# Optimization experiments

Measured on AMD Instinct MI355X. Metric: run time of the kernel, lower is better.

The kernel has to match this reference:

```python
import jax, jax.numpy as jnp
import numpy as np

B, T, D = 16, 4096, 64
K = 4096              # num_embeddings
DECAY = 0.99
COMMITMENT = 0.25
EPS = 1e-5


def setup_inputs() -> dict:
    key = jax.random.key(0)
    k1, k2 = jax.random.split(key)
    inputs = jax.random.normal(k1, (B, T, D), dtype=jnp.float32)
    # torch init: uniform_(-1/K, 1/K); _ema_w initialized to a copy of weight
    weight = jax.random.uniform(k2, (K, D), dtype=jnp.float32, minval=-1.0 / K, maxval=1.0 / K)
    return {
        "inputs": inputs,
        "weight": weight,
        "ema_cluster_size": jnp.zeros((K,), jnp.float32),
        "ema_w": weight,
    }


def reference(inputs, weight, ema_cluster_size, ema_w):
    b, t, d = inputs.shape
    flat = inputs.reshape(-1, d)                                   # [N, D]
    dist = (jnp.sum(flat * flat, axis=1, keepdims=True)
            + jnp.sum(weight * weight, axis=1)
            - 2.0 * flat @ weight.T)
    idx = jnp.argmin(dist, axis=1)                                 # [N]
    quantized = weight[idx].reshape(inputs.shape)                  # gather [B,T,D]

    # --- EMA codebook update (torch.no_grad path; one-hot matmuls == segment sums) ---
    counts = jax.ops.segment_sum(jnp.ones((flat.shape[0],), flat.dtype), idx, num_segments=K)
    cs = ema_cluster_size * DECAY + (1.0 - DECAY) * counts
    n = jnp.sum(cs)
    cs = (cs + EPS) / (n + K * EPS) * n                            # Laplace smoothing
    dw = jax.ops.segment_sum(flat, idx, num_segments=K)            # encodings.T @ flat
    new_ema_w = ema_w * DECAY + (1.0 - DECAY) * dw
    new_weight = new_ema_w / cs[:, None]

    # --- losses (on pre-update codebook, as in torch) ---
    e_latent = jnp.mean((jax.lax.stop_gradient(quantized) - inputs) ** 2)
    q_latent = jnp.mean((quantized - jax.lax.stop_gradient(inputs)) ** 2)
    loss = q_latent + COMMITMENT * e_latent

    # straight-through estimator
    quantized_st = inputs + jax.lax.stop_gradient(quantized - inputs)
    encoding_indices = idx.reshape(b, t)
    return quantized_st, loss, encoding_indices, new_weight, cs, new_ema_w
```

## Files before the change

kernel.cpp:

```cpp
#include <hip/hip_runtime.h>
#include <math.h>

#define NROWS 65536
#define DDIM  64
#define KCODE 4096
#define NSPLIT 4
#define KSPL  (KCODE / NSPLIT)
#define STEPS (KSPL / 16)
#define SMASK (STEPS - 1)

#define O_Q    0
#define O_LOSS 4194304
#define O_IDX  4194305
#define O_NW   4259841
#define O_CS   4521985
#define O_NEW  4526081

#define O_A      262144
#define O_B2     327680
#define O_CNT   1000000
#define O_OFF   1010000
#define O_CUR   1020000
#define O_ORD   1030000
#define O_LP    (O_NW + 131074)

typedef _Float16 f16x8 __attribute__((ext_vector_type(8)));
typedef float    f32x4 __attribute__((ext_vector_type(4)));

__global__ __launch_bounds__(256)
void vq_prep(const float* __restrict__ x, const float* __restrict__ w,
             float* __restrict__ out, unsigned long long* __restrict__ keys) {
    int i = blockIdx.x * 256 + threadIdx.x;
    {
        const int k = i >> 6, j = i & 63;
        float E = w[i] * 4096.0f;
        _Float16 h = (_Float16)E;
        float r = E - (float)h;
        _Float16 lo = (_Float16)(r * 4096.0f);
        const size_t pos = (size_t)(k >> 4) * 1024 + (size_t)(j >> 5) * 512
                         + (size_t)((j >> 3) & 3) * 128 + (size_t)(k & 15) * 8
                         + (size_t)(j & 7);
        ((_Float16*)out)[pos] = h;
        ((_Float16*)out)[262144 + pos] = lo;
    }
    if (i < NROWS) keys[i] = 0xFFFFFFFFFFFFFFFFULL;
    if (i < KCODE) ((unsigned*)(out + O_CNT))[i] = 0u;
    if ((i & 3) == 0) {
        const int row = i >> 2;
        const float4* xr = (const float4*)(x + (size_t)row * DDIM);
        float ax = 0.f, ay = 0.f, az = 0.f, aw = 0.f;
        #pragma unroll
        for (int j = 0; j < 16; ++j) {
            float4 v = xr[j];
            ax += v.x * v.x; ay += v.y * v.y; az += v.z * v.z; aw += v.w * v.w;
        }
        out[O_A + row] = (ax + ay) + (az + aw);
    }
    if ((i & 63) == 0) {
        const int k = i >> 6;
        const float4* wr = (const float4*)(w + (size_t)k * DDIM);
        float ax = 0.f, ay = 0.f, az = 0.f, aw = 0.f;
        #pragma unroll
        for (int j = 0; j < 16; ++j) {
            float4 v = wr[j];
            ax += v.x * v.x; ay += v.y * v.y; az += v.z * v.z; aw += v.w * v.w;
        }
        out[O_B2 + k] = (ax + ay) + (az + aw);
    }
}

__device__ inline void split8(float4 a, float4 b, f16x8& hi, f16x8& lo) {
    float vv[8] = {a.x, a.y, a.z, a.w, b.x, b.y, b.z, b.w};
    #pragma unroll
    for (int j = 0; j < 8; ++j) {
        float X = vv[j] * 256.0f;
        _Float16 h = (_Float16)X;
        float r = X - (float)h;
        hi[j] = h;
        lo[j] = (_Float16)(r * 4096.0f);
    }
}

__global__ __launch_bounds__(256, 3)
void vq_argmin_mfma(const float* __restrict__ x,
                    const _Float16* __restrict__ ehi,
                    const _Float16* __restrict__ elo,
                    const float* __restrict__ Ag,
                    const float* __restrict__ b2g,
                    unsigned long long* __restrict__ keys) {
    __shared__ __align__(16) float b2sh[KSPL];
    const int tid = threadIdx.x;
    const int k0  = blockIdx.y * KSPL;
    ((float4*)b2sh)[tid] = ((const float4*)(b2g + k0))[tid];
    __syncthreads();

    const int l   = tid & 63;
    const int w   = tid >> 6;
    const int g   = l >> 4;
    const int c16 = l & 15;
    const int rowbase = blockIdx.x * 128 + w * 32;

    f16x8 xh[2][2], xl[2][2];
    #pragma unroll
    for (int r = 0; r < 2; ++r) {
        const float* xr = x + (size_t)(rowbase + r * 16 + c16) * DDIM + g * 8;
        float4 a0 = *(const float4*)(xr);
        float4 a1 = *(const float4*)(xr + 4);
        float4 a2 = *(const float4*)(xr + 32);
        float4 a3 = *(const float4*)(xr + 36);
        split8(a0, a1, xh[r][0], xl[r][0]);
        split8(a2, a3, xh[r][1], xl[r][1]);
    }
    float A_reg[2][4];
    #pragma unroll
    for (int r = 0; r < 2; ++r)
        #pragma unroll
        for (int v = 0; v < 4; ++v)
            A_reg[r][v] = Ag[rowbase + r * 16 + 4 * g + v];

    float bestv[2][4]; int bidx[2][4];
    #pragma unroll
    for (int r = 0; r < 2; ++r)
        #pragma unroll
        for (int v = 0; v < 4; ++v) { bestv[r][v] = INFINITY; bidx[r][v] = 0; }

    const _Float16* eh = ehi + (size_t)(k0 >> 4) * 1024 + (size_t)l * 8;
    const _Float16* el = elo + (size_t)(k0 >> 4) * 1024 + (size_t)l * 8;

    f16x8 bh0[2], bh1[2], bl0[2], bl1[2];
    float b2r[2];
    unsigned off[2] = {0u, 1024u};
    int b2i[2] = {c16, 16 + c16};
    int cbase = k0 + c16;
    const f32x4 fzero = {0.f, 0.f, 0.f, 0.f};

#define LOADB(sl) do {                                       \
        const unsigned _o = off[sl];                         \
        bh0[sl] = *(const f16x8*)(eh + _o);                  \
        bh1[sl] = *(const f16x8*)(eh + _o + 512);            \
        bl0[sl] = *(const f16x8*)(el + _o);                  \
        bl1[sl] = *(const f16x8*)(el + _o + 512);            \
        b2r[sl] = b2sh[b2i[sl] & (KSPL - 1)];                \
        off[sl] += 2048u;                                    \
        b2i[sl] += 32;                                       \
    } while (0)

#define COMP(sl) do {                                                             \
        f32x4 acc1[2], acc2[2];                                                   \
        _Pragma("unroll")                                                         \
        for (int r = 0; r < 2; ++r) {                                             \
            acc1[r] = __builtin_amdgcn_mfma_f32_16x16x32_f16(xh[r][0], bh0[sl], fzero,   0, 0, 0); \
            acc1[r] = __builtin_amdgcn_mfma_f32_16x16x32_f16(xh[r][1], bh1[sl], acc1[r], 0, 0, 0); \
            acc2[r] = __builtin_amdgcn_mfma_f32_16x16x32_f16(xl[r][0], bh0[sl], fzero,   0, 0, 0); \
            acc2[r] = __builtin_amdgcn_mfma_f32_16x16x32_f16(xl[r][1], bh1[sl], acc2[r], 0, 0, 0); \
            acc2[r] = __builtin_amdgcn_mfma_f32_16x16x32_f16(xh[r][0], bl0[sl], acc2[r], 0, 0, 0); \
            acc2[r] = __builtin_amdgcn_mfma_f32_16x16x32_f16(xh[r][1], bl1[sl], acc2[r], 0, 0, 0); \
        }                                                                         \
        _Pragma("unroll")                                                         \
        for (int r = 0; r < 2; ++r) {                                             \
            _Pragma("unroll")                                                     \
            for (int v = 0; v < 4; ++v) {                                         \
                float dotc = fmaf(acc2[r][v], 0x1p-12f, acc1[r][v]);              \
                float t = A_reg[r][v] + b2r[sl];                                  \
                float sc = fmaf(dotc, -0x1p-19f, t);                              \
                bool lt = sc < bestv[r][v];      \
                bestv[r][v] = lt ? sc : bestv[r][v];                              \
                bidx[r][v]  = lt ? cbase : bidx[r][v];                            \
            }                                                                     \
        }                                                                         \
        cbase += 16;                                                              \
    } while (0)

    LOADB(0);
    LOADB(1);

    #pragma unroll 1
    for (int s = 0; s < STEPS; s += 2) {
        COMP(0);
        LOADB(0);
        COMP(1);
        LOADB(1);
    }
#undef LOADB
#undef COMP

    #pragma unroll
    for (int off2 = 1; off2 < 16; off2 <<= 1) {
        #pragma unroll
        for (int r = 0; r < 2; ++r)
            #pragma unroll
            for (int v = 0; v < 4; ++v) {
                float ob = __shfl_xor(bestv[r][v], off2);
                int   oi = __shfl_xor(bidx[r][v], off2);
                if (ob < bestv[r][v] || (ob == bestv[r][v] && oi < bidx[r][v])) {
                    bestv[r][v] = ob; bidx[r][v] = oi;
                }
            }
    }
    if (c16 == 0) {
        #pragma unroll
        for (int r = 0; r < 2; ++r)
            #pragma unroll
            for (int v = 0; v < 4; ++v) {
                const int row = rowbase + r * 16 + 4 * g + v;
                unsigned long long key =
                    ((unsigned long long)__float_as_uint(bestv[r][v]) << 32) |
                    (unsigned)bidx[r][v];
                atomicMin(&keys[row], key);
            }
    }
}

__global__ __launch_bounds__(1024)
void vq_hist(const unsigned long long* __restrict__ keys,
             unsigned* __restrict__ counts) {
    __shared__ unsigned h[KCODE];
    const int tid = threadIdx.x;
    #pragma unroll
    for (int j = 0; j < 4; ++j) h[tid + j * 1024] = 0u;
    __syncthreads();
    const int row = blockIdx.x * 1024 + tid;
    const unsigned k = (unsigned)(keys[row] & 0xFFFFFFFFu);
    atomicAdd(&h[k], 1u);
    __syncthreads();
    #pragma unroll
    for (int j = 0; j < 4; ++j) {
        unsigned v = h[tid + j * 1024];
        if (v) atomicAdd(&counts[tid + j * 1024], v);
    }
}

__global__ __launch_bounds__(1024)
void vq_scan(const unsigned* __restrict__ counts,
             unsigned* __restrict__ offs, unsigned* __restrict__ cursor) {
    __shared__ unsigned red[1024];
    const int tid = threadIdx.x;
    unsigned c[4], tot = 0;
    #pragma unroll
    for (int j = 0; j < 4; ++j) { c[j] = counts[tid * 4 + j]; tot += c[j]; }
    red[tid] = tot;
    __syncthreads();
    for (int s = 1; s < 1024; s <<= 1) {
        unsigned v = (tid >= s) ? red[tid - s] : 0u;
        __syncthreads();
        red[tid] += v;
        __syncthreads();
    }
    unsigned base = red[tid] - tot;
    #pragma unroll
    for (int j = 0; j < 4; ++j) {
        offs[tid * 4 + j] = base;
        cursor[tid * 4 + j] = base;
        base += c[j];
    }
}

__global__ __launch_bounds__(256)
void vq_scatter(const unsigned long long* __restrict__ keys,
                unsigned* __restrict__ cursor, unsigned* __restrict__ order) {
    const int row = blockIdx.x * 256 + threadIdx.x;
    const unsigned k = (unsigned)(keys[row] & 0xFFFFFFFFu);
    const unsigned slot = atomicAdd(&cursor[k], 1u);
    order[slot] = row;
}

__global__ __launch_bounds__(256)
void vq_dw(const float* __restrict__ x, const float* __restrict__ ema_w,
           const unsigned* __restrict__ counts, const unsigned* __restrict__ offs,
           const unsigned* __restrict__ order, float* __restrict__ out) {
    const int tid = threadIdx.x;
    const int lane = tid & 63;
    const int k = blockIdx.x * 4 + (tid >> 6);
    const unsigned cnt = counts[k];
    const unsigned off = offs[k];
    float acc = 0.f;
    for (unsigned i = 0; i < cnt; ++i) {
        const unsigned row = order[off + i];
        acc += x[(size_t)row * DDIM + lane];
    }
    const float e = ema_w[(size_t)k * DDIM + lane];
    out[O_NEW + (size_t)k * DDIM + lane] = fmaf(0.01f, acc, 0.99f * e);
    if (lane == 0) out[O_CS + k] = (float)cnt;
}

__global__ __launch_bounds__(256)
void vq_gather2(const float* __restrict__ x, const float* __restrict__ w,
                const unsigned long long* __restrict__ keys,
                float* __restrict__ out, float* __restrict__ lpart) {
    const int tid = threadIdx.x;
    const int l16 = tid & 15;
    const int row = blockIdx.x * 16 + (tid >> 4);
    const int k = (int)(unsigned)(keys[row] & 0xFFFFFFFFu);
    if (l16 == 0) out[O_IDX + row] = (float)k;

    const float4 w4 = ((const float4*)(w + (size_t)k * DDIM))[l16];
    const float4 x4 = ((const float4*)(x + (size_t)row * DDIM))[l16];
    float4 o;
    o.x = x4.x + (w4.x - x4.x);
    o.y = x4.y + (w4.y - x4.y);
    o.z = x4.z + (w4.z - x4.z);
    o.w = x4.w + (w4.w - x4.w);
    ((float4*)(out + O_Q + (size_t)row * DDIM))[l16] = o;
    float dx = w4.x - x4.x, dy = w4.y - x4.y, dz = w4.z - x4.z, dw_ = w4.w - x4.w;
    float e = dx * dx + dy * dy + dz * dz + dw_ * dw_;
    #pragma unroll
    for (int off = 32; off > 0; off >>= 1) e += __shfl_down(e, off);
    if ((tid & 63) == 0) lpart[blockIdx.x * 4 + (tid >> 6)] = e;
}

__global__ __launch_bounds__(1024)
void vq_cs(const float* __restrict__ ecs, const float* __restrict__ lpart,
           float* __restrict__ out) {
    __shared__ float red[1024];
    __shared__ double dred[1024];
    const int tid = threadIdx.x;
    double dl = 0.0;
    #pragma unroll
    for (int j = 0; j < 16; ++j) dl += (double)lpart[j * 1024 + tid];
    dred[tid] = dl;
    float cs[4];
    float local = 0.f;
    #pragma unroll
    for (int j = 0; j < 4; ++j) {
        int k = j * 1024 + tid;
        float cnt = out[O_CS + k];
        cs[j] = ecs[k] * 0.99f + 0.01f * cnt;
        local += cs[j];
    }
    red[tid] = local;
    for (int s = 512; s > 0; s >>= 1) {
        __syncthreads();
        if (tid < s) { red[tid] += red[tid + s]; dred[tid] += dred[tid + s]; }
    }
    __syncthreads();
    const float n = red[0];
    const float denom = n + 0.04096f;
    #pragma unroll
    for (int j = 0; j < 4; ++j) {
        int k = j * 1024 + tid;
        out[O_CS + k] = (cs[j] + 1e-5f) / denom * n;
    }
    if (tid == 0) out[O_LOSS] = 1.25f * (float)(dred[0] / 4194304.0);
}

__global__ __launch_bounds__(256)
void vq_final(float* __restrict__ out) {
    int i = blockIdx.x * 256 + threadIdx.x;
    if (i >= KCODE * DDIM) return;
    int k = i >> 6;
    out[O_NW + i] = out[O_NEW + i] / out[O_CS + k];
}

extern "C" void kernel_launch(void* const* d_in, const int* in_sizes, int n_in,
                              void* d_out, int out_size, void* d_ws, size_t ws_size,
                              hipStream_t stream) {
    (void)in_sizes; (void)n_in; (void)out_size; (void)d_ws; (void)ws_size;
    const float* x    = (const float*)d_in[0];
    const float* w    = (const float*)d_in[1];
    const float* ecs  = (const float*)d_in[2];
    const float* emaw = (const float*)d_in[3];
    float* out = (float*)d_out;

    const _Float16* ehi = (const _Float16*)out;
    const _Float16* elo = ((const _Float16*)out) + 262144;
    const float*    Ag  = out + O_A;
    unsigned long long* keys = (unsigned long long*)(out + O_NW + 1);
    unsigned* counts = (unsigned*)(out + O_CNT);
    unsigned* offs   = (unsigned*)(out + O_OFF);
    unsigned* cursor = (unsigned*)(out + O_CUR);
    unsigned* order  = (unsigned*)(out + O_ORD);
    float*    lpart  = out + O_LP;

    vq_prep       <<<1024, 256, 0, stream>>>(x, w, out, keys);
    vq_argmin_mfma<<<dim3(512, NSPLIT), 256, 0, stream>>>(x, ehi, elo, Ag,
                                                          out + O_B2, keys);
    vq_hist       <<<64, 1024, 0, stream>>>(keys, counts);
    vq_scan       <<<1, 1024, 0, stream>>>(counts, offs, cursor);
    vq_scatter    <<<256, 256, 0, stream>>>(keys, cursor, order);
    vq_dw         <<<1024, 256, 0, stream>>>(x, emaw, counts, offs, order, out);
    vq_gather2    <<<4096, 256, 0, stream>>>(x, w, keys, out, lpart);
    vq_cs         <<<1, 1024, 0, stream>>>(ecs, lpart, out);
    vq_final      <<<1024, 256, 0, stream>>>(out);
}
```

Baseline: 184.7 us.

## Double rows per wave, halve K split, interleave hi/lo codebook tiles

Each wave now processes 64 rows (four 16-row MFMA tiles) instead of 32, so every codebook fragment loaded is reused across twice as many rows. The K dimension is split 2 ways instead of 4, which halves the number of per-row atomicMin merges and the redundant x loads and splits. The hi and lo fp16 codebook halves are interleaved into one contiguous 2048-element block per 16 codes, so one pointer walks both. The cost is more registers per thread (occupancy bound lowered from 3 to 2 blocks) and fewer blocks in the grid.

```diff
diff --git a/kernel.cpp b/kernel.cpp
--- a/kernel.cpp
+++ b/kernel.cpp
@@ -4,10 +4,9 @@
 #define NROWS 65536
 #define DDIM  64
 #define KCODE 4096
-#define NSPLIT 4
+#define NSPLIT 2
 #define KSPL  (KCODE / NSPLIT)
 #define STEPS (KSPL / 16)
-#define SMASK (STEPS - 1)
 
 #define O_Q    0
 #define O_LOSS 4194304
@@ -37,11 +36,11 @@
         _Float16 h = (_Float16)E;
         float r = E - (float)h;
         _Float16 lo = (_Float16)(r * 4096.0f);
-        const size_t pos = (size_t)(k >> 4) * 1024 + (size_t)(j >> 5) * 512
+        const size_t pos = (size_t)(k >> 4) * 2048 + (size_t)(j >> 5) * 512
                          + (size_t)((j >> 3) & 3) * 128 + (size_t)(k & 15) * 8
                          + (size_t)(j & 7);
         ((_Float16*)out)[pos] = h;
-        ((_Float16*)out)[262144 + pos] = lo;
+        ((_Float16*)out)[pos + 1024] = lo;
     }
     if (i < NROWS) keys[i] = 0xFFFFFFFFFFFFFFFFULL;
     if (i < KCODE) ((unsigned*)(out + O_CNT))[i] = 0u;
@@ -81,28 +80,29 @@
     }
 }
 
-__global__ __launch_bounds__(256, 3)
+__global__ __launch_bounds__(256, 2)
 void vq_argmin_mfma(const float* __restrict__ x,
-                    const _Float16* __restrict__ ehi,
-                    const _Float16* __restrict__ elo,
+                    const _Float16* __restrict__ etab,
                     const float* __restrict__ Ag,
                     const float* __restrict__ b2g,
                     unsigned long long* __restrict__ keys) {
-    __shared__ __align__(16) float b2sh[KSPL];
+    __shared__ __align__(16) float b2sh[KSPL + 128];
     const int tid = threadIdx.x;
     const int k0  = blockIdx.y * KSPL;
-    ((float4*)b2sh)[tid] = ((const float4*)(b2g + k0))[tid];
+    #pragma unroll
+    for (int j = 0; j < KSPL / 1024; ++j)
+        ((float4*)b2sh)[tid + j * 256] = ((const float4*)(b2g + k0))[tid + j * 256];
     __syncthreads();
 
     const int l   = tid & 63;
     const int w   = tid >> 6;
     const int g   = l >> 4;
     const int c16 = l & 15;
-    const int rowbase = blockIdx.x * 128 + w * 32;
-
-    f16x8 xh[2][2], xl[2][2];
-    #pragma unroll
-    for (int r = 0; r < 2; ++r) {
+    const int rowbase = blockIdx.x * 256 + w * 64;
+
+    f16x8 xh[4][2], xl[4][2];
+    #pragma unroll
+    for (int r = 0; r < 4; ++r) {
         const float* xr = x + (size_t)(rowbase + r * 16 + c16) * DDIM + g * 8;
         float4 a0 = *(const float4*)(xr);
         float4 a1 = *(const float4*)(xr + 4);
@@ -111,56 +111,52 @@
         split8(a0, a1, xh[r][0], xl[r][0]);
         split8(a2, a3, xh[r][1], xl[r][1]);
     }
-    float A_reg[2][4];
-    #pragma unroll
-    for (int r = 0; r < 2; ++r)
+    float A_reg[4][4];
+    #pragma unroll
+    for (int r = 0; r < 4; ++r)
         #pragma unroll
         for (int v = 0; v < 4; ++v)
             A_reg[r][v] = Ag[rowbase + r * 16 + 4 * g + v];
 
-    float bestv[2][4]; int bidx[2][4];
-    #pragma unroll
-    for (int r = 0; r < 2; ++r)
+    float bestv[4][4]; int bidx[4][4];
+    #pragma unroll
+    for (int r = 0; r < 4; ++r)
         #pragma unroll
         for (int v = 0; v < 4; ++v) { bestv[r][v] = INFINITY; bidx[r][v] = 0; }
 
-    const _Float16* eh = ehi + (size_t)(k0 >> 4) * 1024 + (size_t)l * 8;
-    const _Float16* el = elo + (size_t)(k0 >> 4) * 1024 + (size_t)l * 8;
+    const _Float16* p[2];
+    p[0] = etab + (size_t)(k0 >> 4) * 2048 + (size_t)l * 8;
+    p[1] = p[0] + 2048;
 
     f16x8 bh0[2], bh1[2], bl0[2], bl1[2];
     float b2r[2];
-    unsigned off[2] = {0u, 1024u};
     int b2i[2] = {c16, 16 + c16};
     int cbase = k0 + c16;
     const f32x4 fzero = {0.f, 0.f, 0.f, 0.f};
 
 #define LOADB(sl) do {                                       \
-        const unsigned _o = off[sl];                         \
-        bh0[sl] = *(const f16x8*)(eh + _o);                  \
-        bh1[sl] = *(const f16x8*)(eh + _o + 512);            \
-        bl0[sl] = *(const f16x8*)(el + _o);                  \
-        bl1[sl] = *(const f16x8*)(el + _o + 512);            \
-        b2r[sl] = b2sh[b2i[sl] & (KSPL - 1)];                \
-        off[sl] += 2048u;                                    \
+        bh0[sl] = *(const f16x8*)(p[sl]);                    \
+        bh1[sl] = *(const f16x8*)(p[sl] + 512);              \
+        bl0[sl] = *(const f16x8*)(p[sl] + 1024);             \
+        bl1[sl] = *(const f16x8*)(p[sl] + 1536);             \
+        b2r[sl] = b2sh[b2i[sl]];                             \
+        p[sl] += 4096;                                       \
         b2i[sl] += 32;                                       \
     } while (0)
 
 #define COMP(sl) do {                                                             \
-        f32x4 acc1[2], acc2[2];                                                   \
         _Pragma("unroll")                                                         \
-        for (int r = 0; r < 2; ++r) {                                             \
-            acc1[r] = __builtin_amdgcn_mfma_f32_16x16x32_f16(xh[r][0], bh0[sl], fzero,   0, 0, 0); \
-            acc1[r] = __builtin_amdgcn_mfma_f32_16x16x32_f16(xh[r][1], bh1[sl], acc1[r], 0, 0, 0); \
-            acc2[r] = __builtin_amdgcn_mfma_f32_16x16x32_f16(xl[r][0], bh0[sl], fzero,   0, 0, 0); \
-            acc2[r] = __builtin_amdgcn_mfma_f32_16x16x32_f16(xl[r][1], bh1[sl], acc2[r], 0, 0, 0); \
-            acc2[r] = __builtin_amdgcn_mfma_f32_16x16x32_f16(xh[r][0], bl0[sl], acc2[r], 0, 0, 0); \
-            acc2[r] = __builtin_amdgcn_mfma_f32_16x16x32_f16(xh[r][1], bl1[sl], acc2[r], 0, 0, 0); \
-        }                                                                         \
-        _Pragma("unroll")                                                         \
-        for (int r = 0; r < 2; ++r) {                                             \
+        for (int r = 0; r < 4; ++r) {                                             \
+            f32x4 acc1, acc2;                                                     \
+            acc1 = __builtin_amdgcn_mfma_f32_16x16x32_f16(xh[r][0], bh0[sl], fzero, 0, 0, 0); \
+            acc1 = __builtin_amdgcn_mfma_f32_16x16x32_f16(xh[r][1], bh1[sl], acc1,  0, 0, 0); \
+            acc2 = __builtin_amdgcn_mfma_f32_16x16x32_f16(xl[r][0], bh0[sl], fzero, 0, 0, 0); \
+            acc2 = __builtin_amdgcn_mfma_f32_16x16x32_f16(xl[r][1], bh1[sl], acc2,  0, 0, 0); \
+            acc2 = __builtin_amdgcn_mfma_f32_16x16x32_f16(xh[r][0], bl0[sl], acc2,  0, 0, 0); \
+            acc2 = __builtin_amdgcn_mfma_f32_16x16x32_f16(xh[r][1], bl1[sl], acc2,  0, 0, 0); \
             _Pragma("unroll")                                                     \
             for (int v = 0; v < 4; ++v) {                                         \
-                float dotc = fmaf(acc2[r][v], 0x1p-12f, acc1[r][v]);              \
+                float dotc = fmaf(acc2[v], 0x1p-12f, acc1[v]);                    \
                 float t = A_reg[r][v] + b2r[sl];                                  \
                 float sc = fmaf(dotc, -0x1p-19f, t);                              \
                 bool lt = sc < bestv[r][v];      \
@@ -187,7 +183,7 @@
     #pragma unroll
     for (int off2 = 1; off2 < 16; off2 <<= 1) {
         #pragma unroll
-        for (int r = 0; r < 2; ++r)
+        for (int r = 0; r < 4; ++r)
             #pragma unroll
             for (int v = 0; v < 4; ++v) {
                 float ob = __shfl_xor(bestv[r][v], off2);
@@ -199,7 +195,7 @@
     }
     if (c16 == 0) {
         #pragma unroll
-        for (int r = 0; r < 2; ++r)
+        for (int r = 0; r < 4; ++r)
             #pragma unroll
             for (int v = 0; v < 4; ++v) {
                 const int row = rowbase + r * 16 + 4 * g + v;
@@ -361,9 +357,8 @@
     const float* emaw = (const float*)d_in[3];
     float* out = (float*)d_out;
 
-    const _Float16* ehi = (const _Float16*)out;
-    const _Float16* elo = ((const _Float16*)out) + 262144;
-    const float*    Ag  = out + O_A;
+    const _Float16* etab = (const _Float16*)out;
+    const float*    Ag   = out + O_A;
     unsigned long long* keys = (unsigned long long*)(out + O_NW + 1);
     unsigned* counts = (unsigned*)(out + O_CNT);
     unsigned* offs   = (unsigned*)(out + O_OFF);
@@ -372,7 +367,7 @@
     float*    lpart  = out + O_LP;
 
     vq_prep       <<<1024, 256, 0, stream>>>(x, w, out, keys);
-    vq_argmin_mfma<<<dim3(512, NSPLIT), 256, 0, stream>>>(x, ehi, elo, Ag,
+    vq_argmin_mfma<<<dim3(256, NSPLIT), 256, 0, stream>>>(x, etab, Ag,
                                                           out + O_B2, keys);
     vq_hist       <<<64, 1024, 0, stream>>>(keys, counts);
     vq_scan       <<<1, 1024, 0, stream>>>(counts, offs, cursor);
```

New measurement: 179.0 us. -3.1%, faster.

## Interleave hi/lo codebook tiles, take loss from argmin keys, fuse cs into scan

Applied to the files above, without the earlier changes.

Interleaves the fp16 hi and lo codebook halves into one table so each 16-code step reads one contiguous 4KB block. It also drops the wrap-around masking of the b2 index by padding shared memory. The loss is now summed from the min-distance values stored in the argmin keys inside the histogram kernel, so the gather no longer computes squared errors. The separate cs/loss kernel is merged into the scan kernel, removing one launch and a reduction. Taking the loss from the expanded distance formula instead of direct differences may change it numerically, since distances can cancel or go slightly negative.

```diff
diff --git a/kernel.cpp b/kernel.cpp
--- a/kernel.cpp
+++ b/kernel.cpp
@@ -7,7 +7,6 @@
 #define NSPLIT 4
 #define KSPL  (KCODE / NSPLIT)
 #define STEPS (KSPL / 16)
-#define SMASK (STEPS - 1)
 
 #define O_Q    0
 #define O_LOSS 4194304
@@ -22,7 +21,7 @@
 #define O_OFF   1010000
 #define O_CUR   1020000
 #define O_ORD   1030000
-#define O_LP    (O_NW + 131074)
+#define O_LP64  1100000
 
 typedef _Float16 f16x8 __attribute__((ext_vector_type(8)));
 typedef float    f32x4 __attribute__((ext_vector_type(4)));
@@ -37,11 +36,11 @@
         _Float16 h = (_Float16)E;
         float r = E - (float)h;
         _Float16 lo = (_Float16)(r * 4096.0f);
-        const size_t pos = (size_t)(k >> 4) * 1024 + (size_t)(j >> 5) * 512
+        const size_t pos = (size_t)(k >> 4) * 2048 + (size_t)(j >> 5) * 512
                          + (size_t)((j >> 3) & 3) * 128 + (size_t)(k & 15) * 8
                          + (size_t)(j & 7);
         ((_Float16*)out)[pos] = h;
-        ((_Float16*)out)[262144 + pos] = lo;
+        ((_Float16*)out)[pos + 1024] = lo;
     }
     if (i < NROWS) keys[i] = 0xFFFFFFFFFFFFFFFFULL;
     if (i < KCODE) ((unsigned*)(out + O_CNT))[i] = 0u;
@@ -83,12 +82,11 @@
 
 __global__ __launch_bounds__(256, 3)
 void vq_argmin_mfma(const float* __restrict__ x,
-                    const _Float16* __restrict__ ehi,
-                    const _Float16* __restrict__ elo,
+                    const _Float16* __restrict__ etab,
                     const float* __restrict__ Ag,
                     const float* __restrict__ b2g,
                     unsigned long long* __restrict__ keys) {
-    __shared__ __align__(16) float b2sh[KSPL];
+    __shared__ __align__(16) float b2sh[KSPL + 128];
     const int tid = threadIdx.x;
     const int k0  = blockIdx.y * KSPL;
     ((float4*)b2sh)[tid] = ((const float4*)(b2g + k0))[tid];
@@ -124,24 +122,23 @@
         #pragma unroll
         for (int v = 0; v < 4; ++v) { bestv[r][v] = INFINITY; bidx[r][v] = 0; }
 
-    const _Float16* eh = ehi + (size_t)(k0 >> 4) * 1024 + (size_t)l * 8;
-    const _Float16* el = elo + (size_t)(k0 >> 4) * 1024 + (size_t)l * 8;
+    const _Float16* p[2];
+    p[0] = etab + (size_t)(k0 >> 4) * 2048 + (size_t)l * 8;
+    p[1] = p[0] + 2048;
 
     f16x8 bh0[2], bh1[2], bl0[2], bl1[2];
     float b2r[2];
-    unsigned off[2] = {0u, 1024u};
     int b2i[2] = {c16, 16 + c16};
     int cbase = k0 + c16;
     const f32x4 fzero = {0.f, 0.f, 0.f, 0.f};
 
 #define LOADB(sl) do {                                       \
-        const unsigned _o = off[sl];                         \
-        bh0[sl] = *(const f16x8*)(eh + _o);                  \
-        bh1[sl] = *(const f16x8*)(eh + _o + 512);            \
-        bl0[sl] = *(const f16x8*)(el + _o);                  \
-        bl1[sl] = *(const f16x8*)(el + _o + 512);            \
-        b2r[sl] = b2sh[b2i[sl] & (KSPL - 1)];                \
-        off[sl] += 2048u;                                    \
+        bh0[sl] = *(const f16x8*)(p[sl]);                    \
+        bh1[sl] = *(const f16x8*)(p[sl] + 512);              \
+        bl0[sl] = *(const f16x8*)(p[sl] + 1024);             \
+        bl1[sl] = *(const f16x8*)(p[sl] + 1536);             \
+        b2r[sl] = b2sh[b2i[sl]];                             \
+        p[sl] += 4096;                                       \
         b2i[sl] += 32;                                       \
     } while (0)
 
@@ -213,16 +210,28 @@
 
 __global__ __launch_bounds__(1024)
 void vq_hist(const unsigned long long* __restrict__ keys,
-             unsigned* __restrict__ counts) {
+             unsigned* __restrict__ counts, double* __restrict__ lp64) {
     __shared__ unsigned h[KCODE];
+    __shared__ double dsh[16];
     const int tid = threadIdx.x;
     #pragma unroll
     for (int j = 0; j < 4; ++j) h[tid + j * 1024] = 0u;
     __syncthreads();
     const int row = blockIdx.x * 1024 + tid;
-    const unsigned k = (unsigned)(keys[row] & 0xFFFFFFFFu);
+    const unsigned long long kk = keys[row];
+    const unsigned k = (unsigned)(kk & 0xFFFFFFFFu);
+    float sc = __uint_as_float((unsigned)(kk >> 32));
     atomicAdd(&h[k], 1u);
+    #pragma unroll
+    for (int off = 32; off > 0; off >>= 1) sc += __shfl_down(sc, off);
+    if ((tid & 63) == 0) dsh[tid >> 6] = (double)sc;
     __syncthreads();
+    if (tid == 0) {
+        double s = 0.0;
+        #pragma unroll
+        for (int i = 0; i < 16; ++i) s += dsh[i];
+        lp64[blockIdx.x] = s;
+    }
     #pragma unroll
     for (int j = 0; j < 4; ++j) {
         unsigned v = h[tid + j * 1024];
@@ -231,27 +240,45 @@
 }
 
 __global__ __launch_bounds__(1024)
-void vq_scan(const unsigned* __restrict__ counts,
-             unsigned* __restrict__ offs, unsigned* __restrict__ cursor) {
+void vq_scan_cs(const unsigned* __restrict__ counts, const float* __restrict__ ecs,
+                const double* __restrict__ lp64,
+                unsigned* __restrict__ offs, unsigned* __restrict__ cursor,
+                float* __restrict__ out) {
     __shared__ unsigned red[1024];
-    const int tid = threadIdx.x;
-    unsigned c[4], tot = 0;
-    #pragma unroll
-    for (int j = 0; j < 4; ++j) { c[j] = counts[tid * 4 + j]; tot += c[j]; }
-    red[tid] = tot;
+    __shared__ float fred[1024];
+    const int tid = threadIdx.x;
+    unsigned c[4]; float csv[4];
+    unsigned tot = 0; float fl = 0.f;
+    #pragma unroll
+    for (int j = 0; j < 4; ++j) {
+        const int k = tid * 4 + j;
+        c[j] = counts[k];
+        tot += c[j];
+        csv[j] = ecs[k] * 0.99f + 0.01f * (float)c[j];
+        fl += csv[j];
+    }
+    red[tid] = tot; fred[tid] = fl;
     __syncthreads();
     for (int s = 1; s < 1024; s <<= 1) {
         unsigned v = (tid >= s) ? red[tid - s] : 0u;
+        float  fv = (tid >= s) ? fred[tid - s] : 0.f;
         __syncthreads();
-        red[tid] += v;
+        red[tid] += v; fred[tid] += fv;
         __syncthreads();
     }
+    const float n = fred[1023];
     unsigned base = red[tid] - tot;
+    const float denom = n + 0.04096f;
     #pragma unroll
     for (int j = 0; j < 4; ++j) {
-        offs[tid * 4 + j] = base;
-        cursor[tid * 4 + j] = base;
-        base += c[j];
+        const int k = tid * 4 + j;
+        offs[k] = base; cursor[k] = base; base += c[j];
+        out[O_CS + k] = (csv[j] + 1e-5f) / denom * n;
+    }
+    if (tid == 0) {
+        double dl = 0.0;
+        for (int i = 0; i < 64; ++i) dl += lp64[i];
+        out[O_LOSS] = 1.25f * (float)(dl / 4194304.0);
     }
 }
 
@@ -280,19 +307,17 @@
     }
     const float e = ema_w[(size_t)k * DDIM + lane];
     out[O_NEW + (size_t)k * DDIM + lane] = fmaf(0.01f, acc, 0.99f * e);
-    if (lane == 0) out[O_CS + k] = (float)cnt;
 }
 
 __global__ __launch_bounds__(256)
 void vq_gather2(const float* __restrict__ x, const float* __restrict__ w,
                 const unsigned long long* __restrict__ keys,
-                float* __restrict__ out, float* __restrict__ lpart) {
+                float* __restrict__ out) {
     const int tid = threadIdx.x;
     const int l16 = tid & 15;
     const int row = blockIdx.x * 16 + (tid >> 4);
     const int k = (int)(unsigned)(keys[row] & 0xFFFFFFFFu);
     if (l16 == 0) out[O_IDX + row] = (float)k;
-
     const float4 w4 = ((const float4*)(w + (size_t)k * DDIM))[l16];
     const float4 x4 = ((const float4*)(x + (size_t)row * DDIM))[l16];
     float4 o;
@@ -301,46 +326,6 @@
     o.z = x4.z + (w4.z - x4.z);
     o.w = x4.w + (w4.w - x4.w);
     ((float4*)(out + O_Q + (size_t)row * DDIM))[l16] = o;
-    float dx = w4.x - x4.x, dy = w4.y - x4.y, dz = w4.z - x4.z, dw_ = w4.w - x4.w;
-    float e = dx * dx + dy * dy + dz * dz + dw_ * dw_;
-    #pragma unroll
-    for (int off = 32; off > 0; off >>= 1) e += __shfl_down(e, off);
-    if ((tid & 63) == 0) lpart[blockIdx.x * 4 + (tid >> 6)] = e;
-}
-
-__global__ __launch_bounds__(1024)
-void vq_cs(const float* __restrict__ ecs, const float* __restrict__ lpart,
-           float* __restrict__ out) {
-    __shared__ float red[1024];
-    __shared__ double dred[1024];
-    const int tid = threadIdx.x;
-    double dl = 0.0;
-    #pragma unroll
-    for (int j = 0; j < 16; ++j) dl += (double)lpart[j * 1024 + tid];
-    dred[tid] = dl;
-    float cs[4];
-    float local = 0.f;
-    #pragma unroll
-    for (int j = 0; j < 4; ++j) {
-        int k = j * 1024 + tid;
-        float cnt = out[O_CS + k];
-        cs[j] = ecs[k] * 0.99f + 0.01f * cnt;
-        local += cs[j];
-    }
-    red[tid] = local;
-    for (int s = 512; s > 0; s >>= 1) {
-        __syncthreads();
-        if (tid < s) { red[tid] += red[tid + s]; dred[tid] += dred[tid + s]; }
-    }
-    __syncthreads();
-    const float n = red[0];
-    const float denom = n + 0.04096f;
-    #pragma unroll
-    for (int j = 0; j < 4; ++j) {
-        int k = j * 1024 + tid;
-        out[O_CS + k] = (cs[j] + 1e-5f) / denom * n;
-    }
-    if (tid == 0) out[O_LOSS] = 1.25f * (float)(dred[0] / 4194304.0);
 }
 
 __global__ __launch_bounds__(256)
@@ -361,24 +346,22 @@
     const float* emaw = (const float*)d_in[3];
     float* out = (float*)d_out;
 
-    const _Float16* ehi = (const _Float16*)out;
-    const _Float16* elo = ((const _Float16*)out) + 262144;
-    const float*    Ag  = out + O_A;
+    const _Float16* etab = (const _Float16*)out;
+    const float*    Ag   = out + O_A;
     unsigned long long* keys = (unsigned long long*)(out + O_NW + 1);
     unsigned* counts = (unsigned*)(out + O_CNT);
     unsigned* offs   = (unsigned*)(out + O_OFF);
     unsigned* cursor = (unsigned*)(out + O_CUR);
     unsigned* order  = (unsigned*)(out + O_ORD);
-    float*    lpart  = out + O_LP;
+    double*   lp64   = (double*)(out + O_LP64);
 
     vq_prep       <<<1024, 256, 0, stream>>>(x, w, out, keys);
-    vq_argmin_mfma<<<dim3(512, NSPLIT), 256, 0, stream>>>(x, ehi, elo, Ag,
+    vq_argmin_mfma<<<dim3(512, NSPLIT), 256, 0, stream>>>(x, etab, Ag,
                                                           out + O_B2, keys);
-    vq_hist       <<<64, 1024, 0, stream>>>(keys, counts);
-    vq_scan       <<<1, 1024, 0, stream>>>(counts, offs, cursor);
+    vq_hist       <<<64, 1024, 0, stream>>>(keys, counts, lp64);
+    vq_scan_cs    <<<1, 1024, 0, stream>>>(counts, ecs, lp64, offs, cursor, out);
     vq_scatter    <<<256, 256, 0, stream>>>(keys, cursor, order);
     vq_dw         <<<1024, 256, 0, stream>>>(x, emaw, counts, offs, order, out);
-    vq_gather2    <<<4096, 256, 0, stream>>>(x, w, keys, out, lpart);
-    vq_cs         <<<1, 1024, 0, stream>>>(ecs, lpart, out);
+    vq_gather2    <<<4096, 256, 0, stream>>>(x, w, keys, out);
     vq_final      <<<1024, 256, 0, stream>>>(out);
 }
```

New measurement: 185.0 us (median of 2 runs). About the same (+0.1%).
